# Kernel tuning notes

Hardware: AMD Instinct MI355X
Metric: run time of the kernel (lower is better)

## Reference

```python
import jax, jax.numpy as jnp
import numpy as np

EPS = 1e-06


def setup_inputs() -> dict:
    key = jax.random.key(0)
    k1, k2 = jax.random.split(key)
    B, T, N, D, L = 8, 4096, 9, 512, 32
    sources = jax.random.normal(k1, (B, T, N, D), dtype=jnp.float32)
    queries = jax.random.normal(k2, (L, D), dtype=jnp.float32)
    layer_idx = 5
    return {"sources": sources, "queries": queries, "layer_idx": layer_idx}


def reference(sources, queries, layer_idx):
    # sources: (B, T, N, d) stacked block representations (v_stack)
    # RMSNorm keys (no learnable scale)
    rms = jnp.sqrt(jnp.mean(sources * sources, axis=-1, keepdims=True) + EPS)
    k_stack = sources / rms                      # (B, T, N, d)
    w = queries[layer_idx]                       # (d,)
    scores = jnp.einsum('btnd,d->btn', k_stack, w)   # (B, T, N)
    alpha = jax.nn.softmax(scores, axis=-1)          # (B, T, N)
    h = jnp.einsum('btn,btnd->btd', alpha, sources)  # (B, T, d)
    return h
```

## Files before the change

### kernel.cpp

```cpp
#include <hip/hip_runtime.h>
#include <stdint.h>

static constexpr int D = 512;
static constexpr int N = 9;
static constexpr float EPS = 1e-6f;

__global__ __launch_bounds__(256) void block_attn(
    const float4* __restrict__ src4,
    const float4* __restrict__ q4,
    const int*   __restrict__ layer_idx,
    float4* __restrict__ out4,
    int bt_total)
{
    const int lane = threadIdx.x & 63;
    const int wave = threadIdx.x >> 6;
    const int bt   = blockIdx.x * 4 + wave;
    if (bt >= bt_total) return;

    const int li = layer_idx[0];

    const float4* qp = q4 + (size_t)li * (D / 4);
    const float4 w0 = qp[lane];
    const float4 w1 = qp[64 + lane];

    const float4* p = src4 + (size_t)bt * (N * D / 4) + lane;

    float4 s0[N], s1[N];
    float score[N];

    #pragma unroll
    for (int n = 0; n < N; ++n) {
        const float4 a = p[(size_t)n * (D / 4)];
        const float4 b = p[(size_t)n * (D / 4) + 64];
        s0[n] = a; s1[n] = b;

        float ss = a.x * a.x;
        ss = fmaf(a.y, a.y, ss); ss = fmaf(a.z, a.z, ss); ss = fmaf(a.w, a.w, ss);
        ss = fmaf(b.x, b.x, ss); ss = fmaf(b.y, b.y, ss);
        ss = fmaf(b.z, b.z, ss); ss = fmaf(b.w, b.w, ss);

        float dt = a.x * w0.x;
        dt = fmaf(a.y, w0.y, dt); dt = fmaf(a.z, w0.z, dt); dt = fmaf(a.w, w0.w, dt);
        dt = fmaf(b.x, w1.x, dt); dt = fmaf(b.y, w1.y, dt);
        dt = fmaf(b.z, w1.z, dt); dt = fmaf(b.w, w1.w, dt);

        #pragma unroll
        for (int m = 1; m < 64; m <<= 1) {
            ss += __shfl_xor(ss, m, 64);
            dt += __shfl_xor(dt, m, 64);
        }
        score[n] = dt * rsqrtf(ss * (1.0f / 512.0f) + EPS);
    }

    float mx = score[0];
    #pragma unroll
    for (int n = 1; n < N; ++n) mx = fmaxf(mx, score[n]);
    float asum = 0.f;
    float alpha[N];
    #pragma unroll
    for (int n = 0; n < N; ++n) { alpha[n] = __expf(score[n] - mx); asum += alpha[n]; }
    const float inv = 1.0f / asum;

    float4 h0 = {0.f, 0.f, 0.f, 0.f};
    float4 h1 = {0.f, 0.f, 0.f, 0.f};
    #pragma unroll
    for (int n = 0; n < N; ++n) {
        const float a = alpha[n] * inv;
        h0.x = fmaf(a, s0[n].x, h0.x); h0.y = fmaf(a, s0[n].y, h0.y);
        h0.z = fmaf(a, s0[n].z, h0.z); h0.w = fmaf(a, s0[n].w, h0.w);
        h1.x = fmaf(a, s1[n].x, h1.x); h1.y = fmaf(a, s1[n].y, h1.y);
        h1.z = fmaf(a, s1[n].z, h1.z); h1.w = fmaf(a, s1[n].w, h1.w);
    }

    float4* op = out4 + (size_t)bt * (D / 4);
    op[lane]      = h0;
    op[64 + lane] = h1;
}

extern "C" void kernel_launch(void* const* d_in, const int* in_sizes, int n_in,
                              void* d_out, int out_size, void* d_ws, size_t ws_size,
                              hipStream_t stream) {
    const float4* src = (const float4*)d_in[0];
    const float4* q   = (const float4*)d_in[1];
    const int*    li  = (const int*)d_in[2];
    float4* out = (float4*)d_out;

    const int bt_total = in_sizes[0] / (N * D);
    const int blocks = (bt_total + 3) / 4;
    block_attn<<<blocks, 256, 0, stream>>>(src, q, li, out, bt_total);
}
```

Measured before the change: 775.9 us.

## Reload sources in weighted-sum pass and batch shuffle reductions across rows

Stops keeping all 9 rows of source data in registers. The weighted-sum pass now re-reads them from global memory, which should mostly hit in cache. All 18 cross-lane reductions are interleaved so the shuffles can run in parallel, and launch bounds request 4 blocks per CU to raise occupancy. The host also infers whether input sizes are given in bytes or elements. The cost is a second read of the sources, which may fall back to HBM if the cache does not hold them.

```diff
diff --git a/kernel.cpp b/kernel.cpp
--- a/kernel.cpp
+++ b/kernel.cpp
@@ -1,11 +1,12 @@
 #include <hip/hip_runtime.h>
 #include <stdint.h>
+#include <stddef.h>
 
 static constexpr int D = 512;
 static constexpr int N = 9;
 static constexpr float EPS = 1e-6f;
 
-__global__ __launch_bounds__(256) void block_attn(
+__global__ __launch_bounds__(256, 4) void block_attn(
     const float4* __restrict__ src4,
     const float4* __restrict__ q4,
     const int*   __restrict__ layer_idx,
@@ -18,58 +19,65 @@
     if (bt >= bt_total) return;
 
     const int li = layer_idx[0];
-
     const float4* qp = q4 + (size_t)li * (D / 4);
     const float4 w0 = qp[lane];
     const float4 w1 = qp[64 + lane];
 
-    const float4* p = src4 + (size_t)bt * (N * D / 4) + lane;
+    const float4* p = src4 + (size_t)bt * (size_t)(N * (D / 4)) + lane;
 
-    float4 s0[N], s1[N];
-    float score[N];
+    float ss[N], dt[N];
+#pragma unroll
+    for (int n = 0; n < N; ++n) {
+        const float4 a = p[n * (D / 4)];
+        const float4 b = p[n * (D / 4) + 64];
 
-    #pragma unroll
-    for (int n = 0; n < N; ++n) {
-        const float4 a = p[(size_t)n * (D / 4)];
-        const float4 b = p[(size_t)n * (D / 4) + 64];
-        s0[n] = a; s1[n] = b;
+        float s2 = a.x * a.x;
+        s2 = fmaf(a.y, a.y, s2); s2 = fmaf(a.z, a.z, s2); s2 = fmaf(a.w, a.w, s2);
+        s2 = fmaf(b.x, b.x, s2); s2 = fmaf(b.y, b.y, s2);
+        s2 = fmaf(b.z, b.z, s2); s2 = fmaf(b.w, b.w, s2);
 
-        float ss = a.x * a.x;
-        ss = fmaf(a.y, a.y, ss); ss = fmaf(a.z, a.z, ss); ss = fmaf(a.w, a.w, ss);
-        ss = fmaf(b.x, b.x, ss); ss = fmaf(b.y, b.y, ss);
-        ss = fmaf(b.z, b.z, ss); ss = fmaf(b.w, b.w, ss);
+        float dd = a.x * w0.x;
+        dd = fmaf(a.y, w0.y, dd); dd = fmaf(a.z, w0.z, dd); dd = fmaf(a.w, w0.w, dd);
+        dd = fmaf(b.x, w1.x, dd); dd = fmaf(b.y, w1.y, dd);
+        dd = fmaf(b.z, w1.z, dd); dd = fmaf(b.w, w1.w, dd);
 
-        float dt = a.x * w0.x;
-        dt = fmaf(a.y, w0.y, dt); dt = fmaf(a.z, w0.z, dt); dt = fmaf(a.w, w0.w, dt);
-        dt = fmaf(b.x, w1.x, dt); dt = fmaf(b.y, w1.y, dt);
-        dt = fmaf(b.z, w1.z, dt); dt = fmaf(b.w, w1.w, dt);
-
-        #pragma unroll
-        for (int m = 1; m < 64; m <<= 1) {
-            ss += __shfl_xor(ss, m, 64);
-            dt += __shfl_xor(dt, m, 64);
-        }
-        score[n] = dt * rsqrtf(ss * (1.0f / 512.0f) + EPS);
+        ss[n] = s2; dt[n] = dd;
     }
 
+#pragma unroll
+    for (int m = 1; m < 64; m <<= 1) {
+#pragma unroll
+        for (int n = 0; n < N; ++n) {
+            ss[n] += __shfl_xor(ss[n], m, 64);
+            dt[n] += __shfl_xor(dt[n], m, 64);
+        }
+    }
+
+    float score[N];
+#pragma unroll
+    for (int n = 0; n < N; ++n)
+        score[n] = dt[n] * rsqrtf(ss[n] * (1.0f / 512.0f) + EPS);
+
     float mx = score[0];
-    #pragma unroll
+#pragma unroll
     for (int n = 1; n < N; ++n) mx = fmaxf(mx, score[n]);
     float asum = 0.f;
     float alpha[N];
-    #pragma unroll
+#pragma unroll
     for (int n = 0; n < N; ++n) { alpha[n] = __expf(score[n] - mx); asum += alpha[n]; }
     const float inv = 1.0f / asum;
 
     float4 h0 = {0.f, 0.f, 0.f, 0.f};
     float4 h1 = {0.f, 0.f, 0.f, 0.f};
-    #pragma unroll
+#pragma unroll
     for (int n = 0; n < N; ++n) {
-        const float a = alpha[n] * inv;
-        h0.x = fmaf(a, s0[n].x, h0.x); h0.y = fmaf(a, s0[n].y, h0.y);
-        h0.z = fmaf(a, s0[n].z, h0.z); h0.w = fmaf(a, s0[n].w, h0.w);
-        h1.x = fmaf(a, s1[n].x, h1.x); h1.y = fmaf(a, s1[n].y, h1.y);
-        h1.z = fmaf(a, s1[n].z, h1.z); h1.w = fmaf(a, s1[n].w, h1.w);
+        const float an = alpha[n] * inv;
+        const float4 a = p[n * (D / 4)];
+        const float4 b = p[n * (D / 4) + 64];
+        h0.x = fmaf(an, a.x, h0.x); h0.y = fmaf(an, a.y, h0.y);
+        h0.z = fmaf(an, a.z, h0.z); h0.w = fmaf(an, a.w, h0.w);
+        h1.x = fmaf(an, b.x, h1.x); h1.y = fmaf(an, b.y, h1.y);
+        h1.z = fmaf(an, b.z, h1.z); h1.w = fmaf(an, b.w, h1.w);
     }
 
     float4* op = out4 + (size_t)bt * (D / 4);
@@ -80,12 +88,17 @@
 extern "C" void kernel_launch(void* const* d_in, const int* in_sizes, int n_in,
                               void* d_out, int out_size, void* d_ws, size_t ws_size,
                               hipStream_t stream) {
+    (void)n_in; (void)d_ws; (void)ws_size;
     const float4* src = (const float4*)d_in[0];
     const float4* q   = (const float4*)d_in[1];
     const int*    li  = (const int*)d_in[2];
     float4* out = (float4*)d_out;
 
-    const int bt_total = in_sizes[0] / (N * D);
-    const int blocks = (bt_total + 3) / 4;
-    block_attn<<<blocks, 256, 0, stream>>>(src, q, li, out, bt_total);
+    const bool elem_units = (in_sizes[2] == 1);
+    const long long src_elems = elem_units ? (long long)in_sizes[0]
+                                           : (long long)in_sizes[0] / 4;
+    const long long bt_total = src_elems / (long long)(N * D);
+
+    const int blocks = (int)((bt_total + 3) / 4);
+    block_attn<<<blocks, 256, 0, stream>>>(src, q, li, out, (int)bt_total);
 }
```

Result: slower. 880.9 us (+13.5%).
